# Optimization experiments

Hardware: AMD Instinct MI355X
Metric: run time of the kernel (lower is better)

## Reference

```python
import jax, jax.numpy as jnp
import numpy as np

ALPHA = 0.8  # LeakyReLU negative slope (nn.LeakyReLU(self.alpha))
OUT_DIM = 64
EDGE_DIM = 32


def setup_inputs() -> dict:
    key = jax.random.key(0)
    ks = jax.random.split(key, 6)
    N, S, IN_D = 50000, 16, 128
    xav = lambda k, shp: jax.random.uniform(k, shp, jnp.float32, -1.0, 1.0) * (1.414 * np.sqrt(6.0 / (shp[0] + shp[1])))
    return {
        "input": jax.random.normal(ks[0], (N, IN_D), jnp.float32),
        "neigh_feat": jax.random.normal(ks[1], (N * S, IN_D), jnp.float32),
        "edge_emb": jax.random.normal(ks[2], (N * S, EDGE_DIM), jnp.float32),
        "W": xav(ks[3], (IN_D, OUT_DIM)),
        "W2": xav(ks[4], (IN_D, OUT_DIM)),
        "a": xav(ks[5], (2 * OUT_DIM + EDGE_DIM, 1)),
    }


def reference(input, neigh_feat, edge_emb, W, W2, a):
    N = input.shape[0]
    S = neigh_feat.shape[0] // N
    D = W.shape[1]
    E = edge_emb.shape[1]

    x = input @ W                               # [N, D]
    neighs = (neigh_feat @ W2).reshape(N, S, D)  # [N, S, D]
    ee = edge_emb.reshape(N, S, E)               # [N, S, E]

    # a_input = cat([x_rep, neighs, ee], -1); e = leakyrelu(a_input @ a)
    # Split a to avoid materializing the concatenated [N, S, 2D+E] tensor.
    a_x, a_n, a_e = a[:D, 0], a[D:2 * D, 0], a[2 * D:, 0]
    scores = (x @ a_x)[:, None] + neighs @ a_n + ee @ a_e   # [N, S]
    e = jnp.where(scores > 0, scores, ALPHA * scores)        # LeakyReLU

    attention = jax.nn.softmax(e, axis=1)        # softmax over neighbors
    # dropout is a no-op in eval mode (training=False)

    h_prime = jnp.einsum("ns,nsd->nd", attention, neighs)    # [N, D]
    h_edge = jnp.einsum("ns,nse->ne", attention, ee)         # [N, E]

    # concat_node=True, concat_edge=True, activation=None
    return jnp.concatenate([x, h_prime, h_edge], axis=1)      # [N, 2D+E]
```

## Files before the change

kernel.cpp:

```cpp
#include <hip/hip_runtime.h>
#include <hip/hip_fp16.h>


#define BAR() do {                                              \
    asm volatile("s_waitcnt lgkmcnt(0)" ::: "memory");          \
    __builtin_amdgcn_s_barrier();                               \
    asm volatile("" ::: "memory");                              \
} while (0)

#define GLDS16(gp, lp) __builtin_amdgcn_global_load_lds(                     \
    (const __attribute__((address_space(1))) void*)(gp),                     \
    (__attribute__((address_space(3))) void*)(lp), 16, 0, 0)
#define GLDS4(gp, lp)  __builtin_amdgcn_global_load_lds(                     \
    (const __attribute__((address_space(1))) void*)(gp),                     \
    (__attribute__((address_space(3))) void*)(lp), 4, 0, 0)

__device__ __forceinline__ float dot4(float4 a, float4 b) {
    return fmaf(a.x, b.x, fmaf(a.y, b.y, fmaf(a.z, b.z, a.w * b.w)));
}

__global__ __launch_bounds__(256)
void prep_kernel(const float* __restrict__ W,
                 const float* __restrict__ W2,
                 const float* __restrict__ a,
                 float* __restrict__ ws) {
    const int t = threadIdx.x;
    __shared__ float s_a[160];
    if (t < 160) { float v = a[t]; s_a[t] = v; ws[128 + t] = v; }
    __syncthreads();
    if (t < 128) {
        float p = 0.f, pw = 0.f;
        #pragma unroll
        for (int d = 0; d < 64; d++) {
            p  = fmaf(W2[t * 64 + d], s_a[64 + d], p);
            pw = fmaf(W [t * 64 + d], s_a[d],      pw);
        }
        ws[t] = p;
        ws[288 + t] = pw;
    }
}

__device__ __forceinline__ void dma_node(const float* __restrict__ neigh,
                                         const float* __restrict__ edge,
                                         const float* __restrict__ input,
                                         int node, int lane,
                                         float* ng, float* ee, float* inb) {
    const float* gn = neigh + (size_t)node * 2048;
    #pragma unroll
    for (int i = 0; i < 8; i++) GLDS16(gn + i * 256 + lane * 4, ng + i * 256);
    const float* ge = edge + (size_t)node * 512;
    #pragma unroll
    for (int i = 0; i < 2; i++) GLDS16(ge + i * 256 + lane * 4, ee + i * 256);
    const float* gi = input + (size_t)node * 128;
    #pragma unroll
    for (int i = 0; i < 2; i++) GLDS4(gi + i * 64 + lane, inb + i * 64);
}

__global__ __launch_bounds__(256, 6)
void gat_attn(const float* __restrict__ input,
              const float* __restrict__ neigh,
              const float* __restrict__ edge,
              const float* __restrict__ ws,
              float* __restrict__ out, int N) {
    const int t = threadIdx.x;
    const int q = t >> 6;
    const int lane = t & 63;

    __shared__ __align__(16) float s_w2a[128];
    __shared__ __align__(16) float s_wa[128];
    __shared__ __align__(16) float s_ae[32];
    __shared__ __align__(16) float s_in[2][128];
    __shared__ __align__(16) float s_ng[2][2048];
    __shared__ __align__(16) float s_ee[2][512];
    __shared__ __align__(16) float s_sc[16];

    if (t < 128) { s_w2a[t] = ws[t]; s_wa[t] = ws[288 + t]; }
    else if (t < 160) s_ae[t - 128] = ws[128 + t];

    const int stride = gridDim.x;
    int n = blockIdx.x;
    int cur = 0;

    if (q == 3 && n < N) {
        dma_node(neigh, edge, input, n, lane, s_ng[0], s_ee[0], s_in[0]);
        asm volatile("s_waitcnt vmcnt(0)" ::: "memory");
    }
    BAR();

    for (; n < N; n += stride, cur ^= 1) {
        const int nn = n + stride;
        if (q == 3 && nn < N)
            dma_node(neigh, edge, input, nn, lane,
                     s_ng[cur ^ 1], s_ee[cur ^ 1], s_in[cur ^ 1]);

        {
            const int s = t >> 4, g = t & 15;
            const float4* ng4  = (const float4*)(s_ng[cur] + s * 128);
            const float4* w2a4 = (const float4*)s_w2a;
            const float4* in4  = (const float4*)s_in[cur];
            const float4* wa4  = (const float4*)s_wa;
            float p = dot4(ng4[g], w2a4[g]) + dot4(ng4[g + 16], w2a4[g + 16])
                    + dot4(in4[g], wa4[g]) + dot4(in4[g + 16], wa4[g + 16]);
            if (g < 8)
                p += dot4(((const float4*)(s_ee[cur] + s * 32))[g],
                          ((const float4*)s_ae)[g]);
            #pragma unroll
            for (int off = 8; off; off >>= 1) p += __shfl_down(p, off, 16);
            if (g == 0) s_sc[s] = p;
        }
        BAR();

        if (q == 0) {
            float e[16];
            #pragma unroll
            for (int j = 0; j < 4; j++) {
                const float4 v = ((const float4*)s_sc)[j];
                e[4*j+0] = v.x > 0.f ? v.x : 0.8f * v.x;
                e[4*j+1] = v.y > 0.f ? v.y : 0.8f * v.y;
                e[4*j+2] = v.z > 0.f ? v.z : 0.8f * v.z;
                e[4*j+3] = v.w > 0.f ? v.w : 0.8f * v.w;
            }
            float m[8];
            #pragma unroll
            for (int i = 0; i < 8; i++) m[i] = fmaxf(e[i], e[i + 8]);
            #pragma unroll
            for (int i = 0; i < 4; i++) m[i] = fmaxf(m[i], m[i + 4]);
            const float mx = fmaxf(fmaxf(m[0], m[2]), fmaxf(m[1], m[3]));
            #pragma unroll
            for (int s = 0; s < 16; s++) e[s] = __expf(e[s] - mx);
            float sm[8];
            #pragma unroll
            for (int i = 0; i < 8; i++) sm[i] = e[i] + e[i + 8];
            #pragma unroll
            for (int i = 0; i < 4; i++) sm[i] = sm[i] + sm[i + 4];
            const float sum = (sm[0] + sm[2]) + (sm[1] + sm[3]);
            const float rinv = 1.0f / sum;

            const bool isng = (t < 32);
            const float4* base = isng ? ((const float4*)s_ng[cur] + t)
                                      : ((const float4*)s_ee[cur] + (t & 7));
            const int str = isng ? 32 : 8;
            float4 acc = make_float4(0.f, 0.f, 0.f, 0.f);
            #pragma unroll
            for (int s = 0; s < 16; s++) {
                const float4 v = base[s * str];
                acc.x = fmaf(e[s], v.x, acc.x);
                acc.y = fmaf(e[s], v.y, acc.y);
                acc.z = fmaf(e[s], v.z, acc.z);
                acc.w = fmaf(e[s], v.w, acc.w);
            }
            acc.x *= rinv; acc.y *= rinv; acc.z *= rinv; acc.w *= rinv;
            if (isng) {
                union { __half2 h[2]; float2 f; } u;
                u.h[0] = __floats2half2_rn(acc.x, acc.y);
                u.h[1] = __floats2half2_rn(acc.z, acc.w);
                ((float2*)(out + (size_t)n * 160 + 64))[t] = u.f;
            } else if (t < 40) {
                *(float4*)(out + (size_t)n * 160 + 128 + ((t & 7) << 2)) = acc;
            }
        }
        if (q == 3) asm volatile("s_waitcnt vmcnt(0)" ::: "memory");
        BAR();
    }
}

__global__ __launch_bounds__(256, 2)
void post_gemm(const float* __restrict__ input,
               const float* __restrict__ W,
               const float* __restrict__ W2,
               float* __restrict__ out, int N) {
    const int t = threadIdx.x;
    const int NB = (N + 63) >> 6;
    const bool second = ((int)blockIdx.x >= NB);
    const int rbase = (second ? blockIdx.x - NB : blockIdx.x) << 6;
    const int nrows = min(64, N - rbase);
    const float* Wsrc = second ? W2 : W;
    const int dstcol = second ? 64 : 0;

    __shared__ __align__(16) float sS[64 * 128];
    __shared__ __align__(16) float sW[128 * 64];

    #pragma unroll
    for (int i = 0; i < 8; i++) {
        const int idx = t + i * 256;
        ((float4*)sW)[idx] = ((const float4*)Wsrc)[idx];
    }
    if (!second) {
        #pragma unroll
        for (int i = 0; i < 8; i++) {
            const int idx = t + i * 256;
            const int r = idx >> 5;
            float4 v = make_float4(0.f, 0.f, 0.f, 0.f);
            if (r < nrows)
                v = ((const float4*)(input + (size_t)(rbase + r) * 128))[idx & 31];
            ((float4*)sS)[idx] = v;
        }
    } else {
        #pragma unroll
        for (int i = 0; i < 8; i++) {
            const int idx = t + i * 256;
            const int r = idx >> 5, j = idx & 31;
            float4 v = make_float4(0.f, 0.f, 0.f, 0.f);
            if (r < nrows) {
                union { float2 f; __half2 h[2]; } u;
                u.f = ((const float2*)(out + (size_t)(rbase + r) * 160 + 64))[j];
                const float2 lo = __half22float2(u.h[0]);
                const float2 hi = __half22float2(u.h[1]);
                v = make_float4(lo.x, lo.y, hi.x, hi.y);
            }
            ((float4*)sS)[idx] = v;
        }
    }
    __syncthreads();

    const int r0 = ((t >> 4) & 15) << 2, c0 = (t & 15) << 2;
    float4 acc0 = make_float4(0,0,0,0), acc1 = acc0, acc2 = acc0, acc3 = acc0;
    #pragma unroll 2
    for (int k4 = 0; k4 < 32; k4++) {
        const int k = k4 << 2;
        const float4 a0 = *(const float4*)(sS + (r0 + 0) * 128 + k);
        const float4 a1 = *(const float4*)(sS + (r0 + 1) * 128 + k);
        const float4 a2 = *(const float4*)(sS + (r0 + 2) * 128 + k);
        const float4 a3 = *(const float4*)(sS + (r0 + 3) * 128 + k);
        const float4 w0 = *(const float4*)(sW + (k + 0) * 64 + c0);
        const float4 w1 = *(const float4*)(sW + (k + 1) * 64 + c0);
        const float4 w2 = *(const float4*)(sW + (k + 2) * 64 + c0);
        const float4 w3 = *(const float4*)(sW + (k + 3) * 64 + c0);
        #define MADROW(ACC, A)                                              \
            ACC.x = fmaf(A.x, w0.x, ACC.x); ACC.y = fmaf(A.x, w0.y, ACC.y); \
            ACC.z = fmaf(A.x, w0.z, ACC.z); ACC.w = fmaf(A.x, w0.w, ACC.w); \
            ACC.x = fmaf(A.y, w1.x, ACC.x); ACC.y = fmaf(A.y, w1.y, ACC.y); \
            ACC.z = fmaf(A.y, w1.z, ACC.z); ACC.w = fmaf(A.y, w1.w, ACC.w); \
            ACC.x = fmaf(A.z, w2.x, ACC.x); ACC.y = fmaf(A.z, w2.y, ACC.y); \
            ACC.z = fmaf(A.z, w2.z, ACC.z); ACC.w = fmaf(A.z, w2.w, ACC.w); \
            ACC.x = fmaf(A.w, w3.x, ACC.x); ACC.y = fmaf(A.w, w3.y, ACC.y); \
            ACC.z = fmaf(A.w, w3.z, ACC.z); ACC.w = fmaf(A.w, w3.w, ACC.w);
        MADROW(acc0, a0) MADROW(acc1, a1) MADROW(acc2, a2) MADROW(acc3, a3)
        #undef MADROW
    }
    if (r0 + 0 < nrows) *(float4*)(out + (size_t)(rbase + r0 + 0) * 160 + dstcol + c0) = acc0;
    if (r0 + 1 < nrows) *(float4*)(out + (size_t)(rbase + r0 + 1) * 160 + dstcol + c0) = acc1;
    if (r0 + 2 < nrows) *(float4*)(out + (size_t)(rbase + r0 + 2) * 160 + dstcol + c0) = acc2;
    if (r0 + 3 < nrows) *(float4*)(out + (size_t)(rbase + r0 + 3) * 160 + dstcol + c0) = acc3;
}

extern "C" void kernel_launch(void* const* d_in, const int* in_sizes, int n_in,
                              void* d_out, int out_size, void* d_ws, size_t ws_size,
                              hipStream_t stream) {
    const float* input = (const float*)d_in[0];
    const float* neigh = (const float*)d_in[1];
    const float* edge  = (const float*)d_in[2];
    const float* W     = (const float*)d_in[3];
    const float* W2    = (const float*)d_in[4];
    const float* a     = (const float*)d_in[5];
    float* ws = (float*)d_ws;
    float* out = (float*)d_out;

    const int N = in_sizes[0] / 128;
    const int NB = (N + 63) >> 6;

    prep_kernel<<<1, 256, 0, stream>>>(W, W2, a, ws);
    gat_attn<<<1792, 256, 0, stream>>>(input, neigh, edge, ws, out, N);
    post_gemm<<<2 * NB, 256, 0, stream>>>(input, W, W2, out, N);
}
```

Before: 692.8 us.

## Process two nodes per block iteration and spread softmax aggregation across all warps

The attention kernel now handles a pair of nodes per loop iteration, with double-buffered LDS holding both nodes' neighbor and edge tiles. The input-row score term is computed once per node by the DMA warp instead of being redundantly dotted by every score thread. Softmax and weighted aggregation now use all four warps (two per node, splitting the output columns) instead of one. In exchange, LDS use per block doubles, so occupancy and grid size drop (launch bounds 3, 768 blocks), and the odd-N tail is handled by clamping to N-1.

```diff
diff --git a/kernel.cpp b/kernel.cpp
--- a/kernel.cpp
+++ b/kernel.cpp
@@ -5,7 +5,7 @@
 #define BAR() do {                                              \
     asm volatile("s_waitcnt lgkmcnt(0)" ::: "memory");          \
     __builtin_amdgcn_s_barrier();                               \
-    asm volatile("" ::: "memory");                              \
+    asm volatile("" ::: "memory");                               \
 } while (0)
 
 #define GLDS16(gp, lp) __builtin_amdgcn_global_load_lds(                     \
@@ -56,7 +56,7 @@
     for (int i = 0; i < 2; i++) GLDS4(gi + i * 64 + lane, inb + i * 64);
 }
 
-__global__ __launch_bounds__(256, 6)
+__global__ __launch_bounds__(256, 3)
 void gat_attn(const float* __restrict__ input,
               const float* __restrict__ neigh,
               const float* __restrict__ edge,
@@ -69,52 +69,81 @@
     __shared__ __align__(16) float s_w2a[128];
     __shared__ __align__(16) float s_wa[128];
     __shared__ __align__(16) float s_ae[32];
-    __shared__ __align__(16) float s_in[2][128];
-    __shared__ __align__(16) float s_ng[2][2048];
-    __shared__ __align__(16) float s_ee[2][512];
-    __shared__ __align__(16) float s_sc[16];
+    __shared__ __align__(16) float s_ng[2][2][2048];
+    __shared__ __align__(16) float s_ee[2][2][512];
+    __shared__ __align__(16) float s_in[2][2][128];
+    __shared__ __align__(16) float s_sc[32];
+    __shared__ float s_sx[2];
 
     if (t < 128) { s_w2a[t] = ws[t]; s_wa[t] = ws[288 + t]; }
     else if (t < 160) s_ae[t - 128] = ws[128 + t];
 
+    const int P = (N + 1) >> 1;
     const int stride = gridDim.x;
-    int n = blockIdx.x;
+    int p = blockIdx.x;
     int cur = 0;
 
-    if (q == 3 && n < N) {
-        dma_node(neigh, edge, input, n, lane, s_ng[0], s_ee[0], s_in[0]);
+    if (q == 3 && p < P) {
+        dma_node(neigh, edge, input, 2 * p, lane,
+                 s_ng[0][0], s_ee[0][0], s_in[0][0]);
+        dma_node(neigh, edge, input, min(2 * p + 1, N - 1), lane,
+                 s_ng[0][1], s_ee[0][1], s_in[0][1]);
         asm volatile("s_waitcnt vmcnt(0)" ::: "memory");
     }
     BAR();
 
-    for (; n < N; n += stride, cur ^= 1) {
-        const int nn = n + stride;
-        if (q == 3 && nn < N)
-            dma_node(neigh, edge, input, nn, lane,
-                     s_ng[cur ^ 1], s_ee[cur ^ 1], s_in[cur ^ 1]);
+    for (; p < P; p += stride, cur ^= 1) {
+        const int nA = 2 * p;
+        const int nB = min(2 * p + 1, N - 1);
+        const int pn = p + stride;
+
+        if (q == 3) {
+            if (pn < P) {
+                dma_node(neigh, edge, input, 2 * pn, lane,
+                         s_ng[cur ^ 1][0], s_ee[cur ^ 1][0], s_in[cur ^ 1][0]);
+                dma_node(neigh, edge, input, min(2 * pn + 1, N - 1), lane,
+                         s_ng[cur ^ 1][1], s_ee[cur ^ 1][1], s_in[cur ^ 1][1]);
+            }
+            const float2 ia = ((const float2*)s_in[cur][0])[lane];
+            const float2 ib = ((const float2*)s_in[cur][1])[lane];
+            const float2 w  = ((const float2*)s_wa)[lane];
+            float pa = fmaf(ia.x, w.x, ia.y * w.y);
+            float pb = fmaf(ib.x, w.x, ib.y * w.y);
+            #pragma unroll
+            for (int off = 32; off; off >>= 1) {
+                pa += __shfl_xor(pa, off, 64);
+                pb += __shfl_xor(pb, off, 64);
+            }
+            if (lane == 0) { s_sx[0] = pa; s_sx[1] = pb; }
+        }
 
         {
-            const int s = t >> 4, g = t & 15;
-            const float4* ng4  = (const float4*)(s_ng[cur] + s * 128);
+            const int r = t >> 3, g = t & 7;
+            const int node = r >> 4, s = r & 15;
+            const float4* ng4  = (const float4*)(s_ng[cur][node] + s * 128);
             const float4* w2a4 = (const float4*)s_w2a;
-            const float4* in4  = (const float4*)s_in[cur];
-            const float4* wa4  = (const float4*)s_wa;
-            float p = dot4(ng4[g], w2a4[g]) + dot4(ng4[g + 16], w2a4[g + 16])
-                    + dot4(in4[g], wa4[g]) + dot4(in4[g + 16], wa4[g + 16]);
-            if (g < 8)
-                p += dot4(((const float4*)(s_ee[cur] + s * 32))[g],
-                          ((const float4*)s_ae)[g]);
-            #pragma unroll
-            for (int off = 8; off; off >>= 1) p += __shfl_down(p, off, 16);
-            if (g == 0) s_sc[s] = p;
+            float pp = dot4(ng4[g],      w2a4[g])
+                     + dot4(ng4[g + 8],  w2a4[g + 8])
+                     + dot4(ng4[g + 16], w2a4[g + 16])
+                     + dot4(ng4[g + 24], w2a4[g + 24]);
+            pp += dot4(((const float4*)(s_ee[cur][node] + s * 32))[g],
+                       ((const float4*)s_ae)[g]);
+            pp += __shfl_down(pp, 4, 8);
+            pp += __shfl_down(pp, 2, 8);
+            pp += __shfl_down(pp, 1, 8);
+            if (g == 0) s_sc[r] = pp;
         }
         BAR();
 
-        if (q == 0) {
+        {
+            const int node = q & 1, half = q >> 1;
+            const int n = node ? nB : nA;
+            const float sx = s_sx[node];
             float e[16];
             #pragma unroll
             for (int j = 0; j < 4; j++) {
-                const float4 v = ((const float4*)s_sc)[j];
+                float4 v = ((const float4*)s_sc)[node * 4 + j];
+                v.x += sx; v.y += sx; v.z += sx; v.w += sx;
                 e[4*j+0] = v.x > 0.f ? v.x : 0.8f * v.x;
                 e[4*j+1] = v.y > 0.f ? v.y : 0.8f * v.y;
                 e[4*j+2] = v.z > 0.f ? v.z : 0.8f * v.z;
@@ -133,30 +162,40 @@
             for (int i = 0; i < 8; i++) sm[i] = e[i] + e[i + 8];
             #pragma unroll
             for (int i = 0; i < 4; i++) sm[i] = sm[i] + sm[i + 4];
-            const float sum = (sm[0] + sm[2]) + (sm[1] + sm[3]);
-            const float rinv = 1.0f / sum;
-
-            const bool isng = (t < 32);
-            const float4* base = isng ? ((const float4*)s_ng[cur] + t)
-                                      : ((const float4*)s_ee[cur] + (t & 7));
-            const int str = isng ? 32 : 8;
-            float4 acc = make_float4(0.f, 0.f, 0.f, 0.f);
-            #pragma unroll
-            for (int s = 0; s < 16; s++) {
-                const float4 v = base[s * str];
-                acc.x = fmaf(e[s], v.x, acc.x);
-                acc.y = fmaf(e[s], v.y, acc.y);
-                acc.z = fmaf(e[s], v.z, acc.z);
-                acc.w = fmaf(e[s], v.w, acc.w);
-            }
-            acc.x *= rinv; acc.y *= rinv; acc.z *= rinv; acc.w *= rinv;
-            if (isng) {
-                union { __half2 h[2]; float2 f; } u;
-                u.h[0] = __floats2half2_rn(acc.x, acc.y);
-                u.h[1] = __floats2half2_rn(acc.z, acc.w);
-                ((float2*)(out + (size_t)n * 160 + 64))[t] = u.f;
-            } else if (t < 40) {
-                *(float4*)(out + (size_t)n * 160 + 128 + ((t & 7) << 2)) = acc;
+            const float rinv = 1.0f / ((sm[0] + sm[2]) + (sm[1] + sm[3]));
+
+            if (lane < 20) {
+                const int fc = half * 20 + lane;
+                if (fc < 32) {
+                    const float4* col = (const float4*)s_ng[cur][node] + fc;
+                    float4 acc = make_float4(0.f, 0.f, 0.f, 0.f);
+                    #pragma unroll
+                    for (int s = 0; s < 16; s++) {
+                        const float4 v = col[s * 32];
+                        acc.x = fmaf(e[s], v.x, acc.x);
+                        acc.y = fmaf(e[s], v.y, acc.y);
+                        acc.z = fmaf(e[s], v.z, acc.z);
+                        acc.w = fmaf(e[s], v.w, acc.w);
+                    }
+                    union { __half2 h[2]; float2 f; } u;
+                    u.h[0] = __floats2half2_rn(acc.x * rinv, acc.y * rinv);
+                    u.h[1] = __floats2half2_rn(acc.z * rinv, acc.w * rinv);
+                    ((float2*)(out + (size_t)n * 160 + 64))[fc] = u.f;
+                } else {
+                    const int ec = fc - 32;
+                    const float4* col = (const float4*)s_ee[cur][node] + ec;
+                    float4 acc = make_float4(0.f, 0.f, 0.f, 0.f);
+                    #pragma unroll
+                    for (int s = 0; s < 16; s++) {
+                        const float4 v = col[s * 8];
+                        acc.x = fmaf(e[s], v.x, acc.x);
+                        acc.y = fmaf(e[s], v.y, acc.y);
+                        acc.z = fmaf(e[s], v.z, acc.z);
+                        acc.w = fmaf(e[s], v.w, acc.w);
+                    }
+                    acc.x *= rinv; acc.y *= rinv; acc.z *= rinv; acc.w *= rinv;
+                    *(float4*)(out + (size_t)n * 160 + 128 + (ec << 2)) = acc;
+                }
             }
         }
         if (q == 3) asm volatile("s_waitcnt vmcnt(0)" ::: "memory");
@@ -260,6 +299,6 @@
     const int NB = (N + 63) >> 6;
 
     prep_kernel<<<1, 256, 0, stream>>>(W, W2, a, ws);
-    gat_attn<<<1792, 256, 0, stream>>>(input, neigh, edge, ws, out, N);
+    gat_attn<<<768, 256, 0, stream>>>(input, neigh, edge, ws, out, N);
     post_gemm<<<2 * NB, 256, 0, stream>>>(input, W, W2, out, N);
 }
```

Measured after the change: 661.9 us. 4.5% less time.
